# Optimization experiments

Measured on AMD Instinct MI355X. Metric: run time of the kernel, lower is better.

Reference implementation:

```python
import jax, jax.numpy as jnp
import numpy as np

V, OOV, E, HE, HD, N, S, TD = 50000, 50, 256, 512, 512, 32, 400, 30
PAD_INF = -1e10


def _gru_step(h, x, Wih, Whh, bih, bhh):
    gi = x @ Wih.T + bih            # [N,3H]
    gh = h @ Whh.T + bhh
    ir, iz, inn = jnp.split(gi, 3, axis=-1)
    hr, hz, hn = jnp.split(gh, 3, axis=-1)
    r = jax.nn.sigmoid(ir + hr)
    z = jax.nn.sigmoid(iz + hz)
    n = jnp.tanh(inn + r * hn)
    return (1.0 - z) * n + z * h


def setup_inputs() -> dict:
    key = jax.random.key(0)
    ks = iter(jax.random.split(key, 40))
    def rn(shape, s=0.05):
        return s * jax.random.normal(next(ks), shape, dtype=jnp.float32)
    return {
        "src_ids": jax.random.randint(next(ks), (N, S), 0, V),
        "src_mask": jnp.ones((N, S), jnp.float32),
        "trg_ids": jax.random.randint(next(ks), (N, TD), 0, V),
        "ptr_src_idx": jax.random.randint(next(ks), (N, S), 0, V + OOV),
        "embed": rn((V, E), 0.1),
        "Wih_f": rn((3 * HE, E)), "Whh_f": rn((3 * HE, HE)),
        "bih_f": rn((3 * HE,)), "bhh_f": rn((3 * HE,)),
        "Wih_b": rn((3 * HE, E)), "Whh_b": rn((3 * HE, HE)),
        "bih_b": rn((3 * HE,)), "bhh_b": rn((3 * HE,)),
        "Wih_d": rn((3 * HD, E)), "Whh_d": rn((3 * HD, HD)),
        "bih_d": rn((3 * HD,)), "bhh_d": rn((3 * HD,)),
        "Wk": rn((2 * HE, HD)), "Wd": rn((HD, HD)), "battn": rn((HD,)), "v": rn((HD,)),
        "W1": rn((2 * HE + HD, HD)), "b1": rn((HD,)),
        "W2": rn((HD, V)), "b2": rn((V,)),
        "Wp": rn((2 * HE + HD + E, 1)), "bp": rn((1,)),
    }


def reference(src_ids, src_mask, trg_ids, ptr_src_idx, embed,
              Wih_f, Whh_f, bih_f, bhh_f, Wih_b, Whh_b, bih_b, bhh_b,
              Wih_d, Whh_d, bih_d, bhh_d, Wk, Wd, battn, v,
              W1, b1, W2, b2, Wp, bp):
    n = src_ids.shape[0]
    # ---- bidirectional GRU encoder ----
    xt = jnp.swapaxes(embed[src_ids], 0, 1)        # [S,N,E]
    h0 = jnp.zeros((n, HE), jnp.float32)
    def fstep(h, xi):
        h2 = _gru_step(h, xi, Wih_f, Whh_f, bih_f, bhh_f)
        return h2, h2
    def bstep(h, xi):
        h2 = _gru_step(h, xi, Wih_b, Whh_b, bih_b, bhh_b)
        return h2, h2
    _, hf = jax.lax.scan(fstep, h0, xt)
    _, hb = jax.lax.scan(bstep, h0, xt[::-1])
    enc = jnp.swapaxes(jnp.concatenate([hf, hb[::-1]], axis=-1), 0, 1)  # [N,S,2HE]

    key_proj = enc @ Wk                             # [N,S,HD] precomputed attn keys
    mask_add = (1.0 - src_mask) * PAD_INF           # [N,S]
    rows = jnp.arange(n)[:, None]

    trg_emb = jnp.swapaxes(embed[trg_ids], 0, 1)    # [TD,N,E]
    hd0 = jnp.zeros((n, HD), jnp.float32)

    def dstep(h, xi):
        h = _gru_step(h, xi, Wih_d, Whh_d, bih_d, bhh_d)
        # additive attention
        e = jnp.tanh(key_proj + (h @ Wd + battn)[:, None, :]) @ v + mask_add  # [N,S]
        attn = jax.nn.softmax(e, axis=-1)
        ctx = jnp.einsum('ns,nsd->nd', attn, enc)                # [N,2HE]
        concat = jnp.concatenate([h, ctx], axis=-1)              # [N,2HE+HD]
        gen = jax.nn.softmax((concat @ W1 + b1) @ W2 + b2, axis=-1)  # [N,V]
        gen_ext = jnp.concatenate([gen, jnp.zeros((n, OOV), gen.dtype)], axis=-1)
        p_gen = jax.nn.sigmoid(jnp.concatenate([xi, ctx, h], axis=-1) @ Wp + bp)  # [N,1]
        out = (p_gen * gen_ext).at[rows, ptr_src_idx].add((1.0 - p_gen) * attn)
        return h, out

    _, dists = jax.lax.scan(dstep, hd0, trg_emb)    # [TD,N,V+OOV]
    return jnp.swapaxes(dists, 0, 1)                # [N,TD,V+OOV]
```

## Files before the change

### kernel.cpp

```cpp
#include <hip/hip_runtime.h>
#include <math.h>

#define VSZ 50000
#define OOVN 50
#define VE 50050
#define EMB 256
#define HE 512
#define HD 512
#define NB 32
#define SRC 400
#define TDD 30
#define G3 1536
#define ENC_PER_DIR 128
#define DEC_NBLK 128

__device__ __forceinline__ float sigmf(float x) { return 1.f / (1.f + expf(-x)); }

__global__ __launch_bounds__(256) void transpose_kernel(const float* __restrict__ in,
                                                        float* __restrict__ out,
                                                        int rows, int cols) {
    int idx = blockIdx.x * 256 + threadIdx.x;
    if (idx >= rows * cols) return;
    int r = idx / cols, c = idx % cols;
    out[c * rows + r] = in[idx];
}

__global__ __launch_bounds__(256) void gi_kernel(const int* __restrict__ ids,
                                                 const float* __restrict__ embed,
                                                 const float* __restrict__ WihT,
                                                 const float* __restrict__ bih,
                                                 float* __restrict__ gi, int steps) {
    __shared__ float sx[16][EMB];
    __shared__ int stok[16];
    int tid = threadIdx.x;
    int g0 = blockIdx.x * 16;
    if (tid < 16) {
        int row = g0 + tid;
        int s = row / NB, n = row % NB;
        stok[tid] = ids[n * steps + s];
    }
    __syncthreads();
    for (int r = 0; r < 16; ++r) sx[r][tid] = embed[(size_t)stok[r] * EMB + tid];
    __syncthreads();
    int c = blockIdx.y * 256 + tid;
    float b = bih[c];
    float acc[16];
#pragma unroll
    for (int r = 0; r < 16; ++r) acc[r] = b;
    for (int e = 0; e < EMB; e += 4) {
        float w0 = WihT[(size_t)(e + 0) * G3 + c];
        float w1 = WihT[(size_t)(e + 1) * G3 + c];
        float w2 = WihT[(size_t)(e + 2) * G3 + c];
        float w3 = WihT[(size_t)(e + 3) * G3 + c];
#pragma unroll
        for (int r = 0; r < 16; ++r) {
            float4 x4 = *(const float4*)&sx[r][e];
            acc[r] += x4.x * w0 + x4.y * w1 + x4.z * w2 + x4.w * w3;
        }
    }
#pragma unroll
    for (int r = 0; r < 16; ++r) gi[(size_t)(g0 + r) * G3 + c] = acc[r];
}

__global__ __launch_bounds__(512) void enc_scan_kernel(
    const float* __restrict__ giF, const float* __restrict__ giB,
    const float* __restrict__ WhhF, const float* __restrict__ WhhB,
    const float* __restrict__ bhhF, const float* __restrict__ bhhB,
    float* __restrict__ hF0, float* __restrict__ hF1,
    float* __restrict__ hB0, float* __restrict__ hB1,
    float* __restrict__ enc, unsigned int* __restrict__ flags) {
    const int bid = blockIdx.x;
    const int z = bid >> 7;
    const int b1 = bid & 127;
    const int j0 = b1 * 4;
    const float* gi  = z ? giB : giF;
    const float* Whh = z ? WhhB : WhhF;
    const float* bhh = z ? bhhB : bhhF;
    float* hbuf[2];
    hbuf[0] = z ? hB0 : hF0;
    hbuf[1] = z ? hB1 : hF1;
    unsigned int* fl = flags + (size_t)z * SRC * 128;

    __shared__ float hlds[32 * 576];

    const int tid = threadIdx.x;
    const int jl = tid & 3;
    const int kh = (tid >> 2) & 15;
    const int ng = tid >> 6;
    const int j  = j0 + jl;
    const int kbase = kh * 36;

    float4 wreg[3][8];
#pragma unroll
    for (int g = 0; g < 3; ++g) {
        const float* wp = Whh + (size_t)(g * 512 + j) * 512 + kh * 32;
#pragma unroll
        for (int i = 0; i < 8; ++i) wreg[g][i] = *(const float4*)&wp[i * 4];
    }
    const float bR = bhh[j], bZ = bhh[512 + j], bN = bhh[1024 + j];

    for (int t = 0; t < SRC; ++t) {
        const float* hin = hbuf[t & 1];
        float* hout = hbuf[(t + 1) & 1];
        const int s = z ? (SRC - 1 - t) : t;

        float gpre[12];
        if (kh == 0) {
#pragma unroll
            for (int r = 0; r < 4; ++r) {
                const float* gir = gi + (size_t)(s * NB + ng * 4 + r) * G3 + j;
                gpre[r * 3 + 0] = gir[0];
                gpre[r * 3 + 1] = gir[512];
                gpre[r * 3 + 2] = gir[1024];
            }
        }

        const unsigned long long* hin8 = (const unsigned long long*)hin;
        for (int idx = tid; idx < 32 * 256; idx += 512) {
            unsigned long long uv = __hip_atomic_load(&hin8[idx], __ATOMIC_RELAXED,
                                                      __HIP_MEMORY_SCOPE_AGENT);
            union { unsigned long long u; float f[2]; } cv; cv.u = uv;
            int nn = idx >> 8, kk = (idx & 255) << 1;
            int off = nn * 576 + (kk >> 5) * 36 + (kk & 31);
            hlds[off] = cv.f[0];
            hlds[off + 1] = cv.f[1];
        }
        __syncthreads();

        float aR[4] = {0.f, 0.f, 0.f, 0.f};
        float aZ[4] = {0.f, 0.f, 0.f, 0.f};
        float aN[4] = {0.f, 0.f, 0.f, 0.f};
        const float* h0p = &hlds[(ng * 4 + 0) * 576 + kbase];
        const float* h1p = &hlds[(ng * 4 + 1) * 576 + kbase];
        const float* h2p = &hlds[(ng * 4 + 2) * 576 + kbase];
        const float* h3p = &hlds[(ng * 4 + 3) * 576 + kbase];
#pragma unroll
        for (int i = 0; i < 8; ++i) {
            float4 wr = wreg[0][i], wz = wreg[1][i], wn = wreg[2][i];
            float4 ha = *(const float4*)&h0p[i * 4];
            float4 hb = *(const float4*)&h1p[i * 4];
            float4 hc = *(const float4*)&h2p[i * 4];
            float4 hd = *(const float4*)&h3p[i * 4];
            aR[0] += ha.x*wr.x + ha.y*wr.y + ha.z*wr.z + ha.w*wr.w;
            aZ[0] += ha.x*wz.x + ha.y*wz.y + ha.z*wz.z + ha.w*wz.w;
            aN[0] += ha.x*wn.x + ha.y*wn.y + ha.z*wn.z + ha.w*wn.w;
            aR[1] += hb.x*wr.x + hb.y*wr.y + hb.z*wr.z + hb.w*wr.w;
            aZ[1] += hb.x*wz.x + hb.y*wz.y + hb.z*wz.z + hb.w*wz.w;
            aN[1] += hb.x*wn.x + hb.y*wn.y + hb.z*wn.z + hb.w*wn.w;
            aR[2] += hc.x*wr.x + hc.y*wr.y + hc.z*wr.z + hc.w*wr.w;
            aZ[2] += hc.x*wz.x + hc.y*wz.y + hc.z*wz.z + hc.w*wz.w;
            aN[2] += hc.x*wn.x + hc.y*wn.y + hc.z*wn.z + hc.w*wn.w;
            aR[3] += hd.x*wr.x + hd.y*wr.y + hd.z*wr.z + hd.w*wr.w;
            aZ[3] += hd.x*wz.x + hd.y*wz.y + hd.z*wz.z + hd.w*wz.w;
            aN[3] += hd.x*wn.x + hd.y*wn.y + hd.z*wn.z + hd.w*wn.w;
        }
#pragma unroll
        for (int r = 0; r < 4; ++r) {
            aR[r] += __shfl_xor(aR[r], 4);  aR[r] += __shfl_xor(aR[r], 8);
            aR[r] += __shfl_xor(aR[r], 16); aR[r] += __shfl_xor(aR[r], 32);
            aZ[r] += __shfl_xor(aZ[r], 4);  aZ[r] += __shfl_xor(aZ[r], 8);
            aZ[r] += __shfl_xor(aZ[r], 16); aZ[r] += __shfl_xor(aZ[r], 32);
            aN[r] += __shfl_xor(aN[r], 4);  aN[r] += __shfl_xor(aN[r], 8);
            aN[r] += __shfl_xor(aN[r], 16); aN[r] += __shfl_xor(aN[r], 32);
        }
        if (kh == 0) {
#pragma unroll
            for (int r = 0; r < 4; ++r) {
                int n = ng * 4 + r;
                float rr  = sigmf(gpre[r * 3 + 0] + bR + aR[r]);
                float zz  = sigmf(gpre[r * 3 + 1] + bZ + aZ[r]);
                float nn2 = tanhf(gpre[r * 3 + 2] + bN + rr * aN[r]);
                float hp  = hlds[n * 576 + (j >> 5) * 36 + (j & 31)];
                float hnew = (1.f - zz) * nn2 + zz * hp;
                __hip_atomic_store(&hout[n * 512 + j], hnew, __ATOMIC_RELAXED,
                                   __HIP_MEMORY_SCOPE_AGENT);
                enc[(size_t)(n * SRC + s) * 1024 + z * 512 + j] = hnew;
            }
        }
        __syncthreads();
        if (tid == 0)
            __hip_atomic_store(&fl[t * 128 + b1], 1u, __ATOMIC_RELAXED,
                               __HIP_MEMORY_SCOPE_AGENT);
        if (tid < 64) {
            const unsigned int* ft = fl + t * 128;
            for (;;) {
                unsigned int a = __hip_atomic_load(&ft[tid], __ATOMIC_RELAXED,
                                                   __HIP_MEMORY_SCOPE_AGENT);
                unsigned int b = __hip_atomic_load(&ft[64 + tid], __ATOMIC_RELAXED,
                                                   __HIP_MEMORY_SCOPE_AGENT);
                if (__all(a != 0u && b != 0u)) break;
                __builtin_amdgcn_s_sleep(1);
            }
        }
        __syncthreads();
    }
}

__global__ __launch_bounds__(512) void dec_scan_kernel(
    const float* __restrict__ gi, const float* __restrict__ Whh,
    const float* __restrict__ bhh, const float* __restrict__ h0,
    float* __restrict__ hall, unsigned int* __restrict__ flags) {
    const int b1 = blockIdx.x;
    const int j0 = b1 * 4;
    __shared__ float hlds[32 * 576];
    const int tid = threadIdx.x;
    const int jl = tid & 3;
    const int kh = (tid >> 2) & 15;
    const int ng = tid >> 6;
    const int j  = j0 + jl;
    const int kbase = kh * 36;

    float4 wreg[3][8];
#pragma unroll
    for (int g = 0; g < 3; ++g) {
        const float* wp = Whh + (size_t)(g * 512 + j) * 512 + kh * 32;
#pragma unroll
        for (int i = 0; i < 8; ++i) wreg[g][i] = *(const float4*)&wp[i * 4];
    }
    const float bR = bhh[j], bZ = bhh[512 + j], bN = bhh[1024 + j];

    for (int t = 0; t < TDD; ++t) {
        const float* hin = t ? (hall + (size_t)(t - 1) * NB * 512) : h0;
        float* hout = hall + (size_t)t * NB * 512;

        float gpre[12];
        if (kh == 0) {
#pragma unroll
            for (int r = 0; r < 4; ++r) {
                const float* gir = gi + (size_t)(t * NB + ng * 4 + r) * G3 + j;
                gpre[r * 3 + 0] = gir[0];
                gpre[r * 3 + 1] = gir[512];
                gpre[r * 3 + 2] = gir[1024];
            }
        }

        const unsigned long long* hin8 = (const unsigned long long*)hin;
        for (int idx = tid; idx < 32 * 256; idx += 512) {
            unsigned long long uv = __hip_atomic_load(&hin8[idx], __ATOMIC_RELAXED,
                                                      __HIP_MEMORY_SCOPE_AGENT);
            union { unsigned long long u; float f[2]; } cv; cv.u = uv;
            int nn = idx >> 8, kk = (idx & 255) << 1;
            int off = nn * 576 + (kk >> 5) * 36 + (kk & 31);
            hlds[off] = cv.f[0];
            hlds[off + 1] = cv.f[1];
        }
        __syncthreads();

        float aR[4] = {0.f, 0.f, 0.f, 0.f};
        float aZ[4] = {0.f, 0.f, 0.f, 0.f};
        float aN[4] = {0.f, 0.f, 0.f, 0.f};
        const float* h0p = &hlds[(ng * 4 + 0) * 576 + kbase];
        const float* h1p = &hlds[(ng * 4 + 1) * 576 + kbase];
        const float* h2p = &hlds[(ng * 4 + 2) * 576 + kbase];
        const float* h3p = &hlds[(ng * 4 + 3) * 576 + kbase];
#pragma unroll
        for (int i = 0; i < 8; ++i) {
            float4 wr = wreg[0][i], wz = wreg[1][i], wn = wreg[2][i];
            float4 ha = *(const float4*)&h0p[i * 4];
            float4 hb = *(const float4*)&h1p[i * 4];
            float4 hc = *(const float4*)&h2p[i * 4];
            float4 hd = *(const float4*)&h3p[i * 4];
            aR[0] += ha.x*wr.x + ha.y*wr.y + ha.z*wr.z + ha.w*wr.w;
            aZ[0] += ha.x*wz.x + ha.y*wz.y + ha.z*wz.z + ha.w*wz.w;
            aN[0] += ha.x*wn.x + ha.y*wn.y + ha.z*wn.z + ha.w*wn.w;
            aR[1] += hb.x*wr.x + hb.y*wr.y + hb.z*wr.z + hb.w*wr.w;
            aZ[1] += hb.x*wz.x + hb.y*wz.y + hb.z*wz.z + hb.w*wz.w;
            aN[1] += hb.x*wn.x + hb.y*wn.y + hb.z*wn.z + hb.w*wn.w;
            aR[2] += hc.x*wr.x + hc.y*wr.y + hc.z*wr.z + hc.w*wr.w;
            aZ[2] += hc.x*wz.x + hc.y*wz.y + hc.z*wz.z + hc.w*wz.w;
            aN[2] += hc.x*wn.x + hc.y*wn.y + hc.z*wn.z + hc.w*wn.w;
            aR[3] += hd.x*wr.x + hd.y*wr.y + hd.z*wr.z + hd.w*wr.w;
            aZ[3] += hd.x*wz.x + hd.y*wz.y + hd.z*wz.z + hd.w*wz.w;
            aN[3] += hd.x*wn.x + hd.y*wn.y + hd.z*wn.z + hd.w*wn.w;
        }
#pragma unroll
        for (int r = 0; r < 4; ++r) {
            aR[r] += __shfl_xor(aR[r], 4);  aR[r] += __shfl_xor(aR[r], 8);
            aR[r] += __shfl_xor(aR[r], 16); aR[r] += __shfl_xor(aR[r], 32);
            aZ[r] += __shfl_xor(aZ[r], 4);  aZ[r] += __shfl_xor(aZ[r], 8);
            aZ[r] += __shfl_xor(aZ[r], 16); aZ[r] += __shfl_xor(aZ[r], 32);
            aN[r] += __shfl_xor(aN[r], 4);  aN[r] += __shfl_xor(aN[r], 8);
            aN[r] += __shfl_xor(aN[r], 16); aN[r] += __shfl_xor(aN[r], 32);
        }
        if (kh == 0) {
#pragma unroll
            for (int r = 0; r < 4; ++r) {
                int n = ng * 4 + r;
                float rr  = sigmf(gpre[r * 3 + 0] + bR + aR[r]);
                float zz  = sigmf(gpre[r * 3 + 1] + bZ + aZ[r]);
                float nn2 = tanhf(gpre[r * 3 + 2] + bN + rr * aN[r]);
                float hp  = hlds[n * 576 + (j >> 5) * 36 + (j & 31)];
                float hnew = (1.f - zz) * nn2 + zz * hp;
                __hip_atomic_store(&hout[n * 512 + j], hnew, __ATOMIC_RELAXED,
                                   __HIP_MEMORY_SCOPE_AGENT);
            }
        }
        __syncthreads();
        if (tid == 0)
            __hip_atomic_store(&flags[t * 128 + b1], 1u, __ATOMIC_RELAXED,
                               __HIP_MEMORY_SCOPE_AGENT);
        if (tid < 64) {
            const unsigned int* ft = flags + t * 128;
            for (;;) {
                unsigned int a = __hip_atomic_load(&ft[tid], __ATOMIC_RELAXED,
                                                   __HIP_MEMORY_SCOPE_AGENT);
                unsigned int b = __hip_atomic_load(&ft[64 + tid], __ATOMIC_RELAXED,
                                                   __HIP_MEMORY_SCOPE_AGENT);
                if (__all(a != 0u && b != 0u)) break;
                __builtin_amdgcn_s_sleep(1);
            }
        }
        __syncthreads();
    }
}

__global__ __launch_bounds__(256) void keyproj_kernel(const float* __restrict__ enc,
                                                      const float* __restrict__ Wk,
                                                      float* __restrict__ kp) {
    __shared__ float sx[8][1024];
    int tid = threadIdx.x;
    int g0 = blockIdx.x * 8;
    for (int i = tid; i < 8 * 1024; i += 256)
        sx[i >> 10][i & 1023] = enc[(size_t)(g0 + (i >> 10)) * 1024 + (i & 1023)];
    __syncthreads();
    int c = blockIdx.y * 256 + tid;
    float acc[8];
#pragma unroll
    for (int r = 0; r < 8; ++r) acc[r] = 0.f;
    for (int k = 0; k < 1024; k += 4) {
        float w0 = Wk[(size_t)(k + 0) * 512 + c];
        float w1 = Wk[(size_t)(k + 1) * 512 + c];
        float w2 = Wk[(size_t)(k + 2) * 512 + c];
        float w3 = Wk[(size_t)(k + 3) * 512 + c];
#pragma unroll
        for (int r = 0; r < 8; ++r) {
            float4 x4 = *(const float4*)&sx[r][k];
            acc[r] += x4.x * w0 + x4.y * w1 + x4.z * w2 + x4.w * w3;
        }
    }
#pragma unroll
    for (int r = 0; r < 8; ++r) kp[(size_t)(g0 + r) * 512 + c] = acc[r];
}

__global__ __launch_bounds__(256) void qall_kernel(const float* __restrict__ hall,
                                                   const float* __restrict__ Wd,
                                                   const float* __restrict__ battn,
                                                   float* __restrict__ qall) {
    __shared__ float sx[8][512];
    int tid = threadIdx.x;
    int g0 = blockIdx.x * 8;
    for (int i = tid; i < 8 * 512; i += 256)
        sx[i >> 9][i & 511] = hall[(size_t)(g0 + (i >> 9)) * 512 + (i & 511)];
    __syncthreads();
    int c = blockIdx.y * 256 + tid;
    float b = battn[c];
    float acc[8];
#pragma unroll
    for (int r = 0; r < 8; ++r) acc[r] = b;
    for (int k = 0; k < 512; k += 4) {
        float w0 = Wd[(size_t)(k + 0) * 512 + c];
        float w1 = Wd[(size_t)(k + 1) * 512 + c];
        float w2 = Wd[(size_t)(k + 2) * 512 + c];
        float w3 = Wd[(size_t)(k + 3) * 512 + c];
#pragma unroll
        for (int r = 0; r < 8; ++r) {
            float4 x4 = *(const float4*)&sx[r][k];
            acc[r] += x4.x * w0 + x4.y * w1 + x4.z * w2 + x4.w * w3;
        }
    }
#pragma unroll
    for (int r = 0; r < 8; ++r) qall[(size_t)(g0 + r) * 512 + c] = acc[r];
}

__global__ __launch_bounds__(256) void escoreall_kernel(const float* __restrict__ kp,
                                                        const float* __restrict__ qall,
                                                        const float* __restrict__ vvec,
                                                        const float* __restrict__ mask,
                                                        float* __restrict__ e) {
    __shared__ float sq[512];
    int tid = threadIdx.x;
    int row0 = blockIdx.x * 4;
    int tn = row0 / SRC;
    int n = tn % NB;
    sq[tid] = qall[(size_t)tn * 512 + tid];
    sq[256 + tid] = qall[(size_t)tn * 512 + 256 + tid];
    __syncthreads();
    int w = tid >> 6, lane = tid & 63;
    int row = row0 + w;
    int s = row % SRC;
    const float* kpr = kp + (size_t)(n * SRC + s) * 512;
    float acc = 0.f;
#pragma unroll
    for (int i = 0; i < 8; ++i) {
        int d = lane + i * 64;
        acc += vvec[d] * tanhf(kpr[d] + sq[d]);
    }
    for (int off = 32; off; off >>= 1) acc += __shfl_down(acc, off, 64);
    if (lane == 0) e[row] = acc + (1.f - mask[n * SRC + s]) * (-1e10f);
}

__global__ __launch_bounds__(256) void softmaxS_kernel(float* __restrict__ e) {
    __shared__ float red[256];
    int n = blockIdx.x, tid = threadIdx.x;
    float* row = e + (size_t)n * SRC;
    float m = -3.4e38f;
    for (int s = tid; s < SRC; s += 256) m = fmaxf(m, row[s]);
    red[tid] = m; __syncthreads();
    for (int off = 128; off; off >>= 1) { if (tid < off) red[tid] = fmaxf(red[tid], red[tid + off]); __syncthreads(); }
    m = red[0]; __syncthreads();
    float sum = 0.f;
    for (int s = tid; s < SRC; s += 256) sum += expf(row[s] - m);
    red[tid] = sum; __syncthreads();
    for (int off = 128; off; off >>= 1) { if (tid < off) red[tid] += red[tid + off]; __syncthreads(); }
    float inv = 1.f / red[0]; __syncthreads();
    for (int s = tid; s < SRC; s += 256) row[s] = expf(row[s] - m) * inv;
}

__global__ __launch_bounds__(256) void ctxall_kernel(const float* __restrict__ attn,
                                                     const float* __restrict__ enc,
                                                     float* __restrict__ ctxall) {
    __shared__ float sa[TDD * SRC];
    int n = blockIdx.x, tid = threadIdx.x;
    for (int i = tid; i < TDD * SRC; i += 256) {
        int t = i / SRC, s = i - t * SRC;
        sa[i] = attn[(size_t)(t * NB + n) * SRC + s];
    }
    __syncthreads();
    int d = blockIdx.y * 256 + tid;
    const float* er = enc + (size_t)n * SRC * 1024 + d;
    float acc[TDD];
#pragma unroll
    for (int t = 0; t < TDD; ++t) acc[t] = 0.f;
    for (int s = 0; s < SRC; s += 4) {
        float e0 = er[(size_t)(s + 0) * 1024];
        float e1 = er[(size_t)(s + 1) * 1024];
        float e2 = er[(size_t)(s + 2) * 1024];
        float e3 = er[(size_t)(s + 3) * 1024];
#pragma unroll
        for (int t = 0; t < TDD; ++t) {
            float4 a4 = *(const float4*)&sa[t * SRC + s];
            acc[t] += a4.x * e0 + a4.y * e1 + a4.z * e2 + a4.w * e3;
        }
    }
#pragma unroll
    for (int t = 0; t < TDD; ++t) ctxall[(size_t)(t * NB + n) * 1024 + d] = acc[t];
}

__global__ __launch_bounds__(256) void pgenall_kernel(const int* __restrict__ trg_ids,
                                                      const float* __restrict__ embed,
                                                      const float* __restrict__ ctxall,
                                                      const float* __restrict__ hall,
                                                      const float* __restrict__ Wp,
                                                      const float* __restrict__ bp,
                                                      float* __restrict__ pgenall) {
    __shared__ float red[256];
    int tn = blockIdx.x, tid = threadIdx.x;
    int t = tn / NB, n = tn % NB;
    int tok = trg_ids[n * TDD + t];
    float acc = 0.f;
    for (int i = tid; i < 1792; i += 256) {
        float val;
        if (i < 256) val = embed[(size_t)tok * EMB + i];
        else if (i < 1280) val = ctxall[(size_t)tn * 1024 + (i - 256)];
        else val = hall[(size_t)tn * 512 + (i - 1280)];
        acc += val * Wp[i];
    }
    red[tid] = acc; __syncthreads();
    for (int off = 128; off; off >>= 1) { if (tid < off) red[tid] += red[tid + off]; __syncthreads(); }
    if (tid == 0) pgenall[tn] = 1.f / (1.f + expf(-(red[0] + bp[0])));
}

__global__ __launch_bounds__(256) void hid1all_kernel(const float* __restrict__ hall,
                                                      const float* __restrict__ ctxall,
                                                      const float* __restrict__ W1,
                                                      const float* __restrict__ b1,
                                                      float* __restrict__ hid1all) {
    __shared__ float sc[8][1536];
    int tid = threadIdx.x;
    int g0 = blockIdx.x * 8;
    for (int i = tid; i < 8 * 512; i += 256)
        sc[i >> 9][i & 511] = hall[(size_t)(g0 + (i >> 9)) * 512 + (i & 511)];
    for (int i = tid; i < 8 * 1024; i += 256)
        sc[i >> 10][512 + (i & 1023)] = ctxall[(size_t)(g0 + (i >> 10)) * 1024 + (i & 1023)];
    __syncthreads();
    int c = blockIdx.y * 256 + tid;
    float acc[8];
    float b = b1[c];
#pragma unroll
    for (int r = 0; r < 8; ++r) acc[r] = b;
    for (int k = 0; k < 1536; k += 4) {
        float w0 = W1[(size_t)(k + 0) * 512 + c];
        float w1 = W1[(size_t)(k + 1) * 512 + c];
        float w2 = W1[(size_t)(k + 2) * 512 + c];
        float w3 = W1[(size_t)(k + 3) * 512 + c];
#pragma unroll
        for (int r = 0; r < 8; ++r) {
            float4 x4 = *(const float4*)&sc[r][k];
            acc[r] += x4.x * w0 + x4.y * w1 + x4.z * w2 + x4.w * w3;
        }
    }
#pragma unroll
    for (int r = 0; r < 8; ++r) hid1all[(size_t)(g0 + r) * 512 + c] = acc[r];
}

__global__ __launch_bounds__(256) void logitsall_kernel(const float* __restrict__ hid1,
                                                        const float* __restrict__ W2,
                                                        const float* __restrict__ b2,
                                                        float* __restrict__ logits) {
    __shared__ float sh[32][512];
    int tid = threadIdx.x;
    int r0 = blockIdx.y * 32;
    for (int i = tid; i < 32 * 512; i += 256) sh[i >> 9][i & 511] = hid1[(size_t)r0 * 512 + i];
    __syncthreads();
    int j = blockIdx.x * 256 + tid;
    if (j >= VSZ) return;
    float acc[32];
#pragma unroll
    for (int r = 0; r < 32; ++r) acc[r] = 0.f;
    for (int k = 0; k < 512; k += 4) {
        float w0 = W2[(size_t)(k + 0) * VSZ + j];
        float w1 = W2[(size_t)(k + 1) * VSZ + j];
        float w2 = W2[(size_t)(k + 2) * VSZ + j];
        float w3 = W2[(size_t)(k + 3) * VSZ + j];
#pragma unroll
        for (int r = 0; r < 32; ++r) {
            float4 h4 = *(const float4*)&sh[r][k];
            acc[r] += h4.x * w0 + h4.y * w1 + h4.z * w2 + h4.w * w3;
        }
    }
    float bb = b2[j];
#pragma unroll
    for (int r = 0; r < 32; ++r) logits[(size_t)(r0 + r) * VSZ + j] = acc[r] + bb;
}

__global__ __launch_bounds__(1024) void outall_kernel(const float* __restrict__ logits,
                                                      const float* __restrict__ pgenall,
                                                      float* __restrict__ out) {
    __shared__ float red[1024];
    int tn = blockIdx.x, tid = threadIdx.x;
    int t = tn / NB, n = tn % NB;
    const float* lrow = logits + (size_t)tn * VSZ;
    float m = -3.4e38f;
    for (int j = tid; j < VSZ; j += 1024) m = fmaxf(m, lrow[j]);
    red[tid] = m; __syncthreads();
    for (int off = 512; off; off >>= 1) { if (tid < off) red[tid] = fmaxf(red[tid], red[tid + off]); __syncthreads(); }
    m = red[0]; __syncthreads();
    float sum = 0.f;
    for (int j = tid; j < VSZ; j += 1024) sum += expf(lrow[j] - m);
    red[tid] = sum; __syncthreads();
    for (int off = 512; off; off >>= 1) { if (tid < off) red[tid] += red[tid + off]; __syncthreads(); }
    float inv = pgenall[tn] / red[0];
    float* orow = out + (size_t)(n * TDD + t) * VE;
    for (int j = tid; j < VE; j += 1024) orow[j] = (j < VSZ) ? expf(lrow[j] - m) * inv : 0.f;
}

__global__ __launch_bounds__(256) void scatterall_kernel(const int* __restrict__ ptr,
                                                         const float* __restrict__ attn,
                                                         const float* __restrict__ pgenall,
                                                         float* __restrict__ out) {
    int f = blockIdx.x * 256 + threadIdx.x;
    if (f >= TDD * NB * SRC) return;
    int tn = f / SRC;
    int s = f - tn * SRC;
    int t = tn / NB, n = tn % NB;
    float w = (1.f - pgenall[tn]) * attn[f];
    atomicAdd(&out[(size_t)(n * TDD + t) * VE + ptr[n * SRC + s]], w);
}

extern "C" void kernel_launch(void* const* d_in, const int* in_sizes, int n_in,
                              void* d_out, int out_size, void* d_ws, size_t ws_size,
                              hipStream_t stream) {
    const int*   src_ids  = (const int*)d_in[0];
    const float* src_mask = (const float*)d_in[1];
    const int*   trg_ids  = (const int*)d_in[2];
    const int*   ptr_idx  = (const int*)d_in[3];
    const float* embed    = (const float*)d_in[4];
    const float* Wih_f = (const float*)d_in[5];
    const float* Whh_f = (const float*)d_in[6];
    const float* bih_f = (const float*)d_in[7];
    const float* bhh_f = (const float*)d_in[8];
    const float* Wih_b = (const float*)d_in[9];
    const float* Whh_b = (const float*)d_in[10];
    const float* bih_b = (const float*)d_in[11];
    const float* bhh_b = (const float*)d_in[12];
    const float* Wih_d = (const float*)d_in[13];
    const float* Whh_d = (const float*)d_in[14];
    const float* bih_d = (const float*)d_in[15];
    const float* bhh_d = (const float*)d_in[16];
    const float* Wk    = (const float*)d_in[17];
    const float* Wd    = (const float*)d_in[18];
    const float* battn = (const float*)d_in[19];
    const float* vvec  = (const float*)d_in[20];
    const float* W1    = (const float*)d_in[21];
    const float* b1    = (const float*)d_in[22];
    const float* W2    = (const float*)d_in[23];
    const float* b2    = (const float*)d_in[24];
    const float* Wp    = (const float*)d_in[25];
    const float* bp    = (const float*)d_in[26];
    float* out = (float*)d_out;

    float* w = (float*)d_ws;
    float* WihTf = w; w += 256 * G3;
    float* WihTb = w; w += 256 * G3;
    float* WihTd = w; w += 256 * G3;
    float* giF = w; w += (size_t)SRC * NB * G3;
    float* giB = w; w += (size_t)SRC * NB * G3;
    float* giD = w; w += (size_t)TDD * NB * G3;
    float* enc = w; w += (size_t)NB * SRC * 1024;
    float* kp  = w; w += (size_t)NB * SRC * 512;
    float* hF0 = w; w += NB * HE;
    float* hF1 = w; w += NB * HE;
    float* hB0 = w; w += NB * HE;
    float* hB1 = w; w += NB * HE;
    float* h0d = w; w += NB * HD;
    float* hD_all = w; w += (size_t)TDD * NB * HD;
    float* q_all  = w; w += (size_t)TDD * NB * 512;
    float* e_all  = w; w += (size_t)TDD * NB * SRC;
    float* ctx_all = w; w += (size_t)TDD * NB * 1024;
    float* hid1_all = w; w += (size_t)TDD * NB * 512;
    float* pgen_all = w; w += 1024;
    unsigned int* encflag = (unsigned int*)w; w += 2 * SRC * 128;
    unsigned int* decflag = (unsigned int*)w; w += TDD * 128;
    float* logits_all = giF;

    transpose_kernel<<<(G3 * 256 + 255) / 256, 256, 0, stream>>>(Wih_f, WihTf, G3, 256);
    transpose_kernel<<<(G3 * 256 + 255) / 256, 256, 0, stream>>>(Wih_b, WihTb, G3, 256);
    transpose_kernel<<<(G3 * 256 + 255) / 256, 256, 0, stream>>>(Wih_d, WihTd, G3, 256);

    gi_kernel<<<dim3(SRC * NB / 16, 6), 256, 0, stream>>>(src_ids, embed, WihTf, bih_f, giF, SRC);
    gi_kernel<<<dim3(SRC * NB / 16, 6), 256, 0, stream>>>(src_ids, embed, WihTb, bih_b, giB, SRC);
    gi_kernel<<<dim3(TDD * NB / 16, 6), 256, 0, stream>>>(trg_ids, embed, WihTd, bih_d, giD, TDD);

    hipMemsetAsync(hF0, 0, NB * HE * sizeof(float), stream);
    hipMemsetAsync(hB0, 0, NB * HE * sizeof(float), stream);
    hipMemsetAsync(h0d, 0, NB * HD * sizeof(float), stream);
    hipMemsetAsync(encflag, 0, (2 * SRC * 128 + TDD * 128) * sizeof(unsigned int), stream);

    enc_scan_kernel<<<2 * ENC_PER_DIR, 512, 0, stream>>>(
        giF, giB, Whh_f, Whh_b, bhh_f, bhh_b,
        hF0, hF1, hB0, hB1, enc, encflag);

    keyproj_kernel<<<dim3(NB * SRC / 8, 2), 256, 0, stream>>>(enc, Wk, kp);

    dec_scan_kernel<<<DEC_NBLK, 512, 0, stream>>>(giD, Whh_d, bhh_d, h0d, hD_all, decflag);

    qall_kernel<<<dim3(TDD * NB / 8, 2), 256, 0, stream>>>(hD_all, Wd, battn, q_all);
    escoreall_kernel<<<TDD * NB * SRC / 4, 256, 0, stream>>>(kp, q_all, vvec, src_mask, e_all);
    softmaxS_kernel<<<TDD * NB, 256, 0, stream>>>(e_all);
    ctxall_kernel<<<dim3(NB, 4), 256, 0, stream>>>(e_all, enc, ctx_all);
    pgenall_kernel<<<TDD * NB, 256, 0, stream>>>(trg_ids, embed, ctx_all, hD_all, Wp, bp, pgen_all);
    hid1all_kernel<<<dim3(TDD * NB / 8, 2), 256, 0, stream>>>(hD_all, ctx_all, W1, b1, hid1_all);
    logitsall_kernel<<<dim3((VSZ + 255) / 256, TDD), 256, 0, stream>>>(hid1_all, W2, b2, logits_all);
    outall_kernel<<<TDD * NB, 1024, 0, stream>>>(logits_all, pgen_all, out);
    scatterall_kernel<<<(TDD * NB * SRC + 255) / 256, 256, 0, stream>>>(ptr_idx, e_all, pgen_all, out);
}
```

Before: 7.687 ms.

## Split encoder scan across batch halves, stream recurrent weights, widen keyproj and logits tiles

The encoder scan now runs 512 blocks (two batch halves per direction) instead of 256, each covering 16 batch rows, with per-half flags so the two halves synchronise independently. Recurrent weights are read from global memory each step instead of being kept in registers, and the final step skips the barrier wait. The keyproj and logits GEMM kernels are retiled so each thread computes two output columns, and logits uses 48-row tiles with 512 threads. This aims to add parallelism and reduce register pressure, at the cost of reloading weights from cache every timestep and running more blocks that must be co-resident to avoid deadlock.

```diff
diff --git a/kernel.cpp b/kernel.cpp
--- a/kernel.cpp
+++ b/kernel.cpp
@@ -11,8 +11,6 @@
 #define SRC 400
 #define TDD 30
 #define G3 1536
-#define ENC_PER_DIR 128
-#define DEC_NBLK 128
 
 __device__ __forceinline__ float sigmf(float x) { return 1.f / (1.f + expf(-x)); }
 
@@ -69,20 +67,131 @@
     float* __restrict__ hF0, float* __restrict__ hF1,
     float* __restrict__ hB0, float* __restrict__ hB1,
     float* __restrict__ enc, unsigned int* __restrict__ flags) {
+    const int z = blockIdx.y;
     const int bid = blockIdx.x;
-    const int z = bid >> 7;
-    const int b1 = bid & 127;
-    const int j0 = b1 * 4;
+    const int p = bid >> 1, q = bid & 1;
+    const int j0 = p * 4, n0 = q * 16;
     const float* gi  = z ? giB : giF;
     const float* Whh = z ? WhhB : WhhF;
     const float* bhh = z ? bhhB : bhhF;
     float* hbuf[2];
     hbuf[0] = z ? hB0 : hF0;
     hbuf[1] = z ? hB1 : hF1;
-    unsigned int* fl = flags + (size_t)z * SRC * 128;
-
+    unsigned int* fl = flags + (size_t)z * SRC * 256;
+
+    __shared__ float hlds[16 * 576];
+
+    const int tid = threadIdx.x;
+    const int jl = tid & 3;
+    const int kh = (tid >> 2) & 15;
+    const int ng = tid >> 6;
+    const int j = j0 + jl;
+    const int kbase = kh * 36;
+
+    const float bR = bhh[j], bZ = bhh[512 + j], bN = bhh[1024 + j];
+    const float* wR = Whh + (size_t)(0 * 512 + j) * 512 + kh * 32;
+    const float* wZ = Whh + (size_t)(1 * 512 + j) * 512 + kh * 32;
+    const float* wN = Whh + (size_t)(2 * 512 + j) * 512 + kh * 32;
+
+    for (int t = 0; t < SRC; ++t) {
+        const int s = z ? (SRC - 1 - t) : t;
+        const float* hin = hbuf[t & 1];
+        float* hout = hbuf[(t + 1) & 1];
+
+        float gpre[6];
+        if (kh == 0) {
+#pragma unroll
+            for (int r = 0; r < 2; ++r) {
+                int n = n0 + ng * 2 + r;
+                const float* gir = gi + (size_t)(s * NB + n) * G3 + j;
+                gpre[r * 3 + 0] = gir[0];
+                gpre[r * 3 + 1] = gir[512];
+                gpre[r * 3 + 2] = gir[1024];
+            }
+        }
+
+        const unsigned long long* hin8 = (const unsigned long long*)(hin + n0 * 512);
+        for (int idx = tid; idx < 16 * 256; idx += 512) {
+            unsigned long long uv = __hip_atomic_load(&hin8[idx], __ATOMIC_RELAXED,
+                                                      __HIP_MEMORY_SCOPE_AGENT);
+            union { unsigned long long u; float f[2]; } cv; cv.u = uv;
+            int nn = idx >> 8, kk = (idx & 255) << 1;
+            int off = nn * 576 + (kk >> 5) * 36 + (kk & 31);
+            hlds[off] = cv.f[0];
+            hlds[off + 1] = cv.f[1];
+        }
+        __syncthreads();
+
+        float aR[2] = {0.f, 0.f}, aZ[2] = {0.f, 0.f}, aN[2] = {0.f, 0.f};
+        const float* h0p = &hlds[(ng * 2 + 0) * 576 + kbase];
+        const float* h1p = &hlds[(ng * 2 + 1) * 576 + kbase];
+#pragma unroll
+        for (int i = 0; i < 32; i += 4) {
+            float4 wr = *(const float4*)&wR[i];
+            float4 wz = *(const float4*)&wZ[i];
+            float4 wn = *(const float4*)&wN[i];
+            float4 ha = *(const float4*)&h0p[i];
+            float4 hb = *(const float4*)&h1p[i];
+            aR[0] += ha.x*wr.x + ha.y*wr.y + ha.z*wr.z + ha.w*wr.w;
+            aZ[0] += ha.x*wz.x + ha.y*wz.y + ha.z*wz.z + ha.w*wz.w;
+            aN[0] += ha.x*wn.x + ha.y*wn.y + ha.z*wn.z + ha.w*wn.w;
+            aR[1] += hb.x*wr.x + hb.y*wr.y + hb.z*wr.z + hb.w*wr.w;
+            aZ[1] += hb.x*wz.x + hb.y*wz.y + hb.z*wz.z + hb.w*wz.w;
+            aN[1] += hb.x*wn.x + hb.y*wn.y + hb.z*wn.z + hb.w*wn.w;
+        }
+#pragma unroll
+        for (int r = 0; r < 2; ++r) {
+            aR[r] += __shfl_xor(aR[r], 4);  aR[r] += __shfl_xor(aR[r], 8);
+            aR[r] += __shfl_xor(aR[r], 16); aR[r] += __shfl_xor(aR[r], 32);
+            aZ[r] += __shfl_xor(aZ[r], 4);  aZ[r] += __shfl_xor(aZ[r], 8);
+            aZ[r] += __shfl_xor(aZ[r], 16); aZ[r] += __shfl_xor(aZ[r], 32);
+            aN[r] += __shfl_xor(aN[r], 4);  aN[r] += __shfl_xor(aN[r], 8);
+            aN[r] += __shfl_xor(aN[r], 16); aN[r] += __shfl_xor(aN[r], 32);
+        }
+        if (kh == 0) {
+#pragma unroll
+            for (int r = 0; r < 2; ++r) {
+                int nloc = ng * 2 + r;
+                int n = n0 + nloc;
+                float rr  = sigmf(gpre[r * 3 + 0] + bR + aR[r]);
+                float zz  = sigmf(gpre[r * 3 + 1] + bZ + aZ[r]);
+                float nn2 = tanhf(gpre[r * 3 + 2] + bN + rr * aN[r]);
+                float hp  = hlds[nloc * 576 + (j >> 5) * 36 + (j & 31)];
+                float hnew = (1.f - zz) * nn2 + zz * hp;
+                __hip_atomic_store(&hout[n * 512 + j], hnew, __ATOMIC_RELAXED,
+                                   __HIP_MEMORY_SCOPE_AGENT);
+                enc[(size_t)(n * SRC + s) * 1024 + z * 512 + j] = hnew;
+            }
+        }
+        __syncthreads();
+        if (tid == 0)
+            __hip_atomic_store(&fl[t * 256 + q * 128 + p], 1u, __ATOMIC_RELAXED,
+                               __HIP_MEMORY_SCOPE_AGENT);
+        if (t != SRC - 1) {
+            if (tid < 64) {
+                const unsigned int* ft = fl + t * 256 + q * 128;
+                for (;;) {
+                    unsigned int a = __hip_atomic_load(&ft[tid], __ATOMIC_RELAXED,
+                                                       __HIP_MEMORY_SCOPE_AGENT);
+                    unsigned int b = __hip_atomic_load(&ft[64 + tid], __ATOMIC_RELAXED,
+                                                       __HIP_MEMORY_SCOPE_AGENT);
+                    if (__all(a != 0u && b != 0u)) break;
+                    __builtin_amdgcn_s_sleep(1);
+                }
+            }
+            __syncthreads();
+        }
+    }
+}
+
+__global__ __launch_bounds__(512) void dec_scan_kernel(
+    const float* __restrict__ gi, const float* __restrict__ Whh,
+    const float* __restrict__ bhh, const float* __restrict__ h0,
+    float* __restrict__ hDs, float* __restrict__ hD_all,
+    unsigned int* __restrict__ flags) {
+    const int b1 = blockIdx.x;
+    const int j0 = b1 * 4;
     __shared__ float hlds[32 * 576];
-
     const int tid = threadIdx.x;
     const int jl = tid & 3;
     const int kh = (tid >> 2) & 15;
@@ -90,25 +199,20 @@
     const int j  = j0 + jl;
     const int kbase = kh * 36;
 
-    float4 wreg[3][8];
-#pragma unroll
-    for (int g = 0; g < 3; ++g) {
-        const float* wp = Whh + (size_t)(g * 512 + j) * 512 + kh * 32;
-#pragma unroll
-        for (int i = 0; i < 8; ++i) wreg[g][i] = *(const float4*)&wp[i * 4];
-    }
     const float bR = bhh[j], bZ = bhh[512 + j], bN = bhh[1024 + j];
-
-    for (int t = 0; t < SRC; ++t) {
-        const float* hin = hbuf[t & 1];
-        float* hout = hbuf[(t + 1) & 1];
-        const int s = z ? (SRC - 1 - t) : t;
+    const float* wR = Whh + (size_t)(0 * 512 + j) * 512 + kh * 32;
+    const float* wZ = Whh + (size_t)(1 * 512 + j) * 512 + kh * 32;
+    const float* wN = Whh + (size_t)(2 * 512 + j) * 512 + kh * 32;
+
+    for (int t = 0; t < TDD; ++t) {
+        const float* hin = t ? (hDs + (size_t)(t - 1) * NB * 512) : h0;
+        float* hout = hDs + (size_t)t * NB * 512;
 
         float gpre[12];
         if (kh == 0) {
 #pragma unroll
             for (int r = 0; r < 4; ++r) {
-                const float* gir = gi + (size_t)(s * NB + ng * 4 + r) * G3 + j;
+                const float* gir = gi + (size_t)(t * NB + ng * 4 + r) * G3 + j;
                 gpre[r * 3 + 0] = gir[0];
                 gpre[r * 3 + 1] = gir[512];
                 gpre[r * 3 + 2] = gir[1024];
@@ -135,12 +239,14 @@
         const float* h2p = &hlds[(ng * 4 + 2) * 576 + kbase];
         const float* h3p = &hlds[(ng * 4 + 3) * 576 + kbase];
 #pragma unroll
-        for (int i = 0; i < 8; ++i) {
-            float4 wr = wreg[0][i], wz = wreg[1][i], wn = wreg[2][i];
-            float4 ha = *(const float4*)&h0p[i * 4];
-            float4 hb = *(const float4*)&h1p[i * 4];
-            float4 hc = *(const float4*)&h2p[i * 4];
-            float4 hd = *(const float4*)&h3p[i * 4];
+        for (int i = 0; i < 32; i += 4) {
+            float4 wr = *(const float4*)&wR[i];
+            float4 wz = *(const float4*)&wZ[i];
+            float4 wn = *(const float4*)&wN[i];
+            float4 ha = *(const float4*)&h0p[i];
+            float4 hb = *(const float4*)&h1p[i];
+            float4 hc = *(const float4*)&h2p[i];
+            float4 hd = *(const float4*)&h3p[i];
             aR[0] += ha.x*wr.x + ha.y*wr.y + ha.z*wr.z + ha.w*wr.w;
             aZ[0] += ha.x*wz.x + ha.y*wz.y + ha.z*wz.z + ha.w*wz.w;
             aN[0] += ha.x*wn.x + ha.y*wn.y + ha.z*wn.z + ha.w*wn.w;
@@ -174,143 +280,27 @@
                 float hnew = (1.f - zz) * nn2 + zz * hp;
                 __hip_atomic_store(&hout[n * 512 + j], hnew, __ATOMIC_RELAXED,
                                    __HIP_MEMORY_SCOPE_AGENT);
-                enc[(size_t)(n * SRC + s) * 1024 + z * 512 + j] = hnew;
-            }
-        }
-        __syncthreads();
-        if (tid == 0)
-            __hip_atomic_store(&fl[t * 128 + b1], 1u, __ATOMIC_RELAXED,
-                               __HIP_MEMORY_SCOPE_AGENT);
-        if (tid < 64) {
-            const unsigned int* ft = fl + t * 128;
-            for (;;) {
-                unsigned int a = __hip_atomic_load(&ft[tid], __ATOMIC_RELAXED,
-                                                   __HIP_MEMORY_SCOPE_AGENT);
-                unsigned int b = __hip_atomic_load(&ft[64 + tid], __ATOMIC_RELAXED,
-                                                   __HIP_MEMORY_SCOPE_AGENT);
-                if (__all(a != 0u && b != 0u)) break;
-                __builtin_amdgcn_s_sleep(1);
-            }
-        }
-        __syncthreads();
-    }
-}
-
-__global__ __launch_bounds__(512) void dec_scan_kernel(
-    const float* __restrict__ gi, const float* __restrict__ Whh,
-    const float* __restrict__ bhh, const float* __restrict__ h0,
-    float* __restrict__ hall, unsigned int* __restrict__ flags) {
-    const int b1 = blockIdx.x;
-    const int j0 = b1 * 4;
-    __shared__ float hlds[32 * 576];
-    const int tid = threadIdx.x;
-    const int jl = tid & 3;
-    const int kh = (tid >> 2) & 15;
-    const int ng = tid >> 6;
-    const int j  = j0 + jl;
-    const int kbase = kh * 36;
-
-    float4 wreg[3][8];
-#pragma unroll
-    for (int g = 0; g < 3; ++g) {
-        const float* wp = Whh + (size_t)(g * 512 + j) * 512 + kh * 32;
-#pragma unroll
-        for (int i = 0; i < 8; ++i) wreg[g][i] = *(const float4*)&wp[i * 4];
-    }
-    const float bR = bhh[j], bZ = bhh[512 + j], bN = bhh[1024 + j];
-
-    for (int t = 0; t < TDD; ++t) {
-        const float* hin = t ? (hall + (size_t)(t - 1) * NB * 512) : h0;
-        float* hout = hall + (size_t)t * NB * 512;
-
-        float gpre[12];
-        if (kh == 0) {
-#pragma unroll
-            for (int r = 0; r < 4; ++r) {
-                const float* gir = gi + (size_t)(t * NB + ng * 4 + r) * G3 + j;
-                gpre[r * 3 + 0] = gir[0];
-                gpre[r * 3 + 1] = gir[512];
-                gpre[r * 3 + 2] = gir[1024];
-            }
-        }
-
-        const unsigned long long* hin8 = (const unsigned long long*)hin;
-        for (int idx = tid; idx < 32 * 256; idx += 512) {
-            unsigned long long uv = __hip_atomic_load(&hin8[idx], __ATOMIC_RELAXED,
-                                                      __HIP_MEMORY_SCOPE_AGENT);
-            union { unsigned long long u; float f[2]; } cv; cv.u = uv;
-            int nn = idx >> 8, kk = (idx & 255) << 1;
-            int off = nn * 576 + (kk >> 5) * 36 + (kk & 31);
-            hlds[off] = cv.f[0];
-            hlds[off + 1] = cv.f[1];
-        }
-        __syncthreads();
-
-        float aR[4] = {0.f, 0.f, 0.f, 0.f};
-        float aZ[4] = {0.f, 0.f, 0.f, 0.f};
-        float aN[4] = {0.f, 0.f, 0.f, 0.f};
-        const float* h0p = &hlds[(ng * 4 + 0) * 576 + kbase];
-        const float* h1p = &hlds[(ng * 4 + 1) * 576 + kbase];
-        const float* h2p = &hlds[(ng * 4 + 2) * 576 + kbase];
-        const float* h3p = &hlds[(ng * 4 + 3) * 576 + kbase];
-#pragma unroll
-        for (int i = 0; i < 8; ++i) {
-            float4 wr = wreg[0][i], wz = wreg[1][i], wn = wreg[2][i];
-            float4 ha = *(const float4*)&h0p[i * 4];
-            float4 hb = *(const float4*)&h1p[i * 4];
-            float4 hc = *(const float4*)&h2p[i * 4];
-            float4 hd = *(const float4*)&h3p[i * 4];
-            aR[0] += ha.x*wr.x + ha.y*wr.y + ha.z*wr.z + ha.w*wr.w;
-            aZ[0] += ha.x*wz.x + ha.y*wz.y + ha.z*wz.z + ha.w*wz.w;
-            aN[0] += ha.x*wn.x + ha.y*wn.y + ha.z*wn.z + ha.w*wn.w;
-            aR[1] += hb.x*wr.x + hb.y*wr.y + hb.z*wr.z + hb.w*wr.w;
-            aZ[1] += hb.x*wz.x + hb.y*wz.y + hb.z*wz.z + hb.w*wz.w;
-            aN[1] += hb.x*wn.x + hb.y*wn.y + hb.z*wn.z + hb.w*wn.w;
-            aR[2] += hc.x*wr.x + hc.y*wr.y + hc.z*wr.z + hc.w*wr.w;
-            aZ[2] += hc.x*wz.x + hc.y*wz.y + hc.z*wz.z + hc.w*wz.w;
-            aN[2] += hc.x*wn.x + hc.y*wn.y + hc.z*wn.z + hc.w*wn.w;
-            aR[3] += hd.x*wr.x + hd.y*wr.y + hd.z*wr.z + hd.w*wr.w;
-            aZ[3] += hd.x*wz.x + hd.y*wz.y + hd.z*wz.z + hd.w*wz.w;
-            aN[3] += hd.x*wn.x + hd.y*wn.y + hd.z*wn.z + hd.w*wn.w;
-        }
-#pragma unroll
-        for (int r = 0; r < 4; ++r) {
-            aR[r] += __shfl_xor(aR[r], 4);  aR[r] += __shfl_xor(aR[r], 8);
-            aR[r] += __shfl_xor(aR[r], 16); aR[r] += __shfl_xor(aR[r], 32);
-            aZ[r] += __shfl_xor(aZ[r], 4);  aZ[r] += __shfl_xor(aZ[r], 8);
-            aZ[r] += __shfl_xor(aZ[r], 16); aZ[r] += __shfl_xor(aZ[r], 32);
-            aN[r] += __shfl_xor(aN[r], 4);  aN[r] += __shfl_xor(aN[r], 8);
-            aN[r] += __shfl_xor(aN[r], 16); aN[r] += __shfl_xor(aN[r], 32);
-        }
-        if (kh == 0) {
-#pragma unroll
-            for (int r = 0; r < 4; ++r) {
-                int n = ng * 4 + r;
-                float rr  = sigmf(gpre[r * 3 + 0] + bR + aR[r]);
-                float zz  = sigmf(gpre[r * 3 + 1] + bZ + aZ[r]);
-                float nn2 = tanhf(gpre[r * 3 + 2] + bN + rr * aN[r]);
-                float hp  = hlds[n * 576 + (j >> 5) * 36 + (j & 31)];
-                float hnew = (1.f - zz) * nn2 + zz * hp;
-                __hip_atomic_store(&hout[n * 512 + j], hnew, __ATOMIC_RELAXED,
-                                   __HIP_MEMORY_SCOPE_AGENT);
+                hD_all[(size_t)t * NB * 512 + n * 512 + j] = hnew;
             }
         }
         __syncthreads();
         if (tid == 0)
             __hip_atomic_store(&flags[t * 128 + b1], 1u, __ATOMIC_RELAXED,
                                __HIP_MEMORY_SCOPE_AGENT);
-        if (tid < 64) {
-            const unsigned int* ft = flags + t * 128;
-            for (;;) {
-                unsigned int a = __hip_atomic_load(&ft[tid], __ATOMIC_RELAXED,
-                                                   __HIP_MEMORY_SCOPE_AGENT);
-                unsigned int b = __hip_atomic_load(&ft[64 + tid], __ATOMIC_RELAXED,
-                                                   __HIP_MEMORY_SCOPE_AGENT);
-                if (__all(a != 0u && b != 0u)) break;
-                __builtin_amdgcn_s_sleep(1);
+        if (t != TDD - 1) {
+            if (tid < 64) {
+                const unsigned int* ft = flags + t * 128;
+                for (;;) {
+                    unsigned int a = __hip_atomic_load(&ft[tid], __ATOMIC_RELAXED,
+                                                       __HIP_MEMORY_SCOPE_AGENT);
+                    unsigned int b = __hip_atomic_load(&ft[64 + tid], __ATOMIC_RELAXED,
+                                                       __HIP_MEMORY_SCOPE_AGENT);
+                    if (__all(a != 0u && b != 0u)) break;
+                    __builtin_amdgcn_s_sleep(1);
+                }
             }
-        }
-        __syncthreads();
+            __syncthreads();
+        }
     }
 }
 
@@ -323,23 +313,25 @@
     for (int i = tid; i < 8 * 1024; i += 256)
         sx[i >> 10][i & 1023] = enc[(size_t)(g0 + (i >> 10)) * 1024 + (i & 1023)];
     __syncthreads();
-    int c = blockIdx.y * 256 + tid;
-    float acc[8];
-#pragma unroll
-    for (int r = 0; r < 8; ++r) acc[r] = 0.f;
+    int c = tid * 2;
+    float acc[8][2];
+#pragma unroll
+    for (int r = 0; r < 8; ++r) { acc[r][0] = 0.f; acc[r][1] = 0.f; }
     for (int k = 0; k < 1024; k += 4) {
-        float w0 = Wk[(size_t)(k + 0) * 512 + c];
-        float w1 = Wk[(size_t)(k + 1) * 512 + c];
-        float w2 = Wk[(size_t)(k + 2) * 512 + c];
-        float w3 = Wk[(size_t)(k + 3) * 512 + c];
+        float2 w0 = *(const float2*)&Wk[(size_t)(k + 0) * 512 + c];
+        float2 w1 = *(const float2*)&Wk[(size_t)(k + 1) * 512 + c];
+        float2 w2 = *(const float2*)&Wk[(size_t)(k + 2) * 512 + c];
+        float2 w3 = *(const float2*)&Wk[(size_t)(k + 3) * 512 + c];
 #pragma unroll
         for (int r = 0; r < 8; ++r) {
             float4 x4 = *(const float4*)&sx[r][k];
-            acc[r] += x4.x * w0 + x4.y * w1 + x4.z * w2 + x4.w * w3;
-        }
-    }
-#pragma unroll
-    for (int r = 0; r < 8; ++r) kp[(size_t)(g0 + r) * 512 + c] = acc[r];
+            acc[r][0] += x4.x * w0.x + x4.y * w1.x + x4.z * w2.x + x4.w * w3.x;
+            acc[r][1] += x4.x * w0.y + x4.y * w1.y + x4.z * w2.y + x4.w * w3.y;
+        }
+    }
+#pragma unroll
+    for (int r = 0; r < 8; ++r)
+        *(float2*)&kp[(size_t)(g0 + r) * 512 + c] = make_float2(acc[r][0], acc[r][1]);
 }
 
 __global__ __launch_bounds__(256) void qall_kernel(const float* __restrict__ hall,
@@ -503,34 +495,36 @@
     for (int r = 0; r < 8; ++r) hid1all[(size_t)(g0 + r) * 512 + c] = acc[r];
 }
 
-__global__ __launch_bounds__(256) void logitsall_kernel(const float* __restrict__ hid1,
+__global__ __launch_bounds__(512) void logitsall_kernel(const float* __restrict__ hid1,
                                                         const float* __restrict__ W2,
                                                         const float* __restrict__ b2,
                                                         float* __restrict__ logits) {
-    __shared__ float sh[32][512];
+    __shared__ float sh[48][512];
     int tid = threadIdx.x;
-    int r0 = blockIdx.y * 32;
-    for (int i = tid; i < 32 * 512; i += 256) sh[i >> 9][i & 511] = hid1[(size_t)r0 * 512 + i];
-    __syncthreads();
-    int j = blockIdx.x * 256 + tid;
+    int r0 = blockIdx.y * 48;
+    for (int i = tid; i < 48 * 512; i += 512) sh[i >> 9][i & 511] = hid1[(size_t)r0 * 512 + i];
+    __syncthreads();
+    int j = blockIdx.x * 1024 + tid * 2;
     if (j >= VSZ) return;
-    float acc[32];
-#pragma unroll
-    for (int r = 0; r < 32; ++r) acc[r] = 0.f;
-    for (int k = 0; k < 512; k += 4) {
-        float w0 = W2[(size_t)(k + 0) * VSZ + j];
-        float w1 = W2[(size_t)(k + 1) * VSZ + j];
-        float w2 = W2[(size_t)(k + 2) * VSZ + j];
-        float w3 = W2[(size_t)(k + 3) * VSZ + j];
-#pragma unroll
-        for (int r = 0; r < 32; ++r) {
-            float4 h4 = *(const float4*)&sh[r][k];
-            acc[r] += h4.x * w0 + h4.y * w1 + h4.z * w2 + h4.w * w3;
-        }
-    }
-    float bb = b2[j];
-#pragma unroll
-    for (int r = 0; r < 32; ++r) logits[(size_t)(r0 + r) * VSZ + j] = acc[r] + bb;
+    float acc[48][2];
+#pragma unroll
+    for (int r = 0; r < 48; ++r) { acc[r][0] = 0.f; acc[r][1] = 0.f; }
+    for (int k = 0; k < 512; k += 2) {
+        float2 w0 = *(const float2*)&W2[(size_t)(k + 0) * VSZ + j];
+        float2 w1 = *(const float2*)&W2[(size_t)(k + 1) * VSZ + j];
+#pragma unroll
+        for (int r = 0; r < 48; ++r) {
+            float2 h2 = *(const float2*)&sh[r][k];
+            acc[r][0] += h2.x * w0.x + h2.y * w1.x;
+            acc[r][1] += h2.x * w0.y + h2.y * w1.y;
+        }
+    }
+    float2 bb = *(const float2*)&b2[j];
+#pragma unroll
+    for (int r = 0; r < 48; ++r) {
+        float2 o; o.x = acc[r][0] + bb.x; o.y = acc[r][1] + bb.y;
+        *(float2*)&logits[(size_t)(r0 + r) * VSZ + j] = o;
+    }
 }
 
 __global__ __launch_bounds__(1024) void outall_kernel(const float* __restrict__ logits,
@@ -541,17 +535,17 @@
     int t = tn / NB, n = tn % NB;
     const float* lrow = logits + (size_t)tn * VSZ;
     float m = -3.4e38f;
-    for (int j = tid; j < VSZ; j += 1024) m = fmaxf(m, lrow[j]);
+    for (int jj = tid; jj < VSZ; jj += 1024) m = fmaxf(m, lrow[jj]);
     red[tid] = m; __syncthreads();
     for (int off = 512; off; off >>= 1) { if (tid < off) red[tid] = fmaxf(red[tid], red[tid + off]); __syncthreads(); }
     m = red[0]; __syncthreads();
     float sum = 0.f;
-    for (int j = tid; j < VSZ; j += 1024) sum += expf(lrow[j] - m);
+    for (int jj = tid; jj < VSZ; jj += 1024) sum += expf(lrow[jj] - m);
     red[tid] = sum; __syncthreads();
     for (int off = 512; off; off >>= 1) { if (tid < off) red[tid] += red[tid + off]; __syncthreads(); }
     float inv = pgenall[tn] / red[0];
     float* orow = out + (size_t)(n * TDD + t) * VE;
-    for (int j = tid; j < VE; j += 1024) orow[j] = (j < VSZ) ? expf(lrow[j] - m) * inv : 0.f;
+    for (int jj = tid; jj < VE; jj += 1024) orow[jj] = (jj < VSZ) ? expf(lrow[jj] - m) * inv : 0.f;
 }
 
 __global__ __launch_bounds__(256) void scatterall_kernel(const int* __restrict__ ptr,
@@ -605,7 +599,7 @@
     float* WihTd = w; w += 256 * G3;
     float* giF = w; w += (size_t)SRC * NB * G3;
     float* giB = w; w += (size_t)SRC * NB * G3;
-    float* giD = w; w += (size_t)TDD * NB * G3;
+    float* giD = w; w += (size_t)SRC * NB * G3;
     float* enc = w; w += (size_t)NB * SRC * 1024;
     float* kp  = w; w += (size_t)NB * SRC * 512;
     float* hF0 = w; w += NB * HE;
@@ -613,13 +607,14 @@
     float* hB0 = w; w += NB * HE;
     float* hB1 = w; w += NB * HE;
     float* h0d = w; w += NB * HD;
+    float* hDs = w; w += (size_t)TDD * NB * HD;
     float* hD_all = w; w += (size_t)TDD * NB * HD;
     float* q_all  = w; w += (size_t)TDD * NB * 512;
     float* e_all  = w; w += (size_t)TDD * NB * SRC;
     float* ctx_all = w; w += (size_t)TDD * NB * 1024;
     float* hid1_all = w; w += (size_t)TDD * NB * 512;
     float* pgen_all = w; w += 1024;
-    unsigned int* encflag = (unsigned int*)w; w += 2 * SRC * 128;
+    unsigned int* encflag = (unsigned int*)w; w += 2 * SRC * 256;
     unsigned int* decflag = (unsigned int*)w; w += TDD * 128;
     float* logits_all = giF;
 
@@ -634,15 +629,15 @@
     hipMemsetAsync(hF0, 0, NB * HE * sizeof(float), stream);
     hipMemsetAsync(hB0, 0, NB * HE * sizeof(float), stream);
     hipMemsetAsync(h0d, 0, NB * HD * sizeof(float), stream);
-    hipMemsetAsync(encflag, 0, (2 * SRC * 128 + TDD * 128) * sizeof(unsigned int), stream);
-
-    enc_scan_kernel<<<2 * ENC_PER_DIR, 512, 0, stream>>>(
+    hipMemsetAsync(encflag, 0, (2 * SRC * 256 + TDD * 128) * sizeof(unsigned int), stream);
+
+    enc_scan_kernel<<<dim3(256, 2), 512, 0, stream>>>(
         giF, giB, Whh_f, Whh_b, bhh_f, bhh_b,
         hF0, hF1, hB0, hB1, enc, encflag);
 
-    keyproj_kernel<<<dim3(NB * SRC / 8, 2), 256, 0, stream>>>(enc, Wk, kp);
-
-    dec_scan_kernel<<<DEC_NBLK, 512, 0, stream>>>(giD, Whh_d, bhh_d, h0d, hD_all, decflag);
+    keyproj_kernel<<<NB * SRC / 8, 256, 0, stream>>>(enc, Wk, kp);
+
+    dec_scan_kernel<<<128, 512, 0, stream>>>(giD, Whh_d, bhh_d, h0d, hDs, hD_all, decflag);
 
     qall_kernel<<<dim3(TDD * NB / 8, 2), 256, 0, stream>>>(hD_all, Wd, battn, q_all);
     escoreall_kernel<<<TDD * NB * SRC / 4, 256, 0, stream>>>(kp, q_all, vvec, src_mask, e_all);
@@ -650,7 +645,7 @@
     ctxall_kernel<<<dim3(NB, 4), 256, 0, stream>>>(e_all, enc, ctx_all);
     pgenall_kernel<<<TDD * NB, 256, 0, stream>>>(trg_ids, embed, ctx_all, hD_all, Wp, bp, pgen_all);
     hid1all_kernel<<<dim3(TDD * NB / 8, 2), 256, 0, stream>>>(hD_all, ctx_all, W1, b1, hid1_all);
-    logitsall_kernel<<<dim3((VSZ + 255) / 256, TDD), 256, 0, stream>>>(hid1_all, W2, b2, logits_all);
+    logitsall_kernel<<<dim3((VSZ + 1023) / 1024, TDD * NB / 48), 512, 0, stream>>>(hid1_all, W2, b2, logits_all);
     outall_kernel<<<TDD * NB, 1024, 0, stream>>>(logits_all, pgen_all, out);
     scatterall_kernel<<<(TDD * NB * SRC + 255) / 256, 256, 0, stream>>>(ptr_idx, e_all, pgen_all, out);
 }
```

Measured after the change: 8.877 ms. 15.5% more time.
